# Kernel optimization log

Measured on AMD Instinct MI355X. Metric: run time of the kernel, lower is better.

## Reference

```python
import jax, jax.numpy as jnp
import numpy as np


def setup_inputs() -> dict:
    key = jax.random.key(0)
    k1, k2 = jax.random.split(key)
    x = jax.random.normal(k1, (4, 2048, 512), dtype=jnp.float32)
    proxy = jax.random.normal(k2, (16, 512), dtype=jnp.float32)
    return {"x": x, "proxy": proxy}


def reference(x, proxy):
    # x: (B, S, D), proxy: (P, D)
    num_proxies = proxy.shape[0]
    # prods: (B, P, S) = proxy @ x^T per batch
    prods = jnp.einsum('pd,bsd->bps', proxy, x)
    # broadcast outer product: (B, P, S, D), then running prefix sum over seq
    y = jnp.cumsum(prods[..., None] * x[:, None, :, :], axis=2)
    # softmax gate over proxies (dim=1), scaled by sqrt(P)
    w = jax.nn.softmax(prods / jnp.sqrt(jnp.float32(num_proxies)), axis=1)
    # weighted sum over proxies -> (B, S, D)
    out = jnp.einsum('bps,bpsd->bsd', w, y)
    return out
```

## Files before the change

### kernel.cpp

```cpp
#include <hip/hip_runtime.h>
#include <hip/hip_bf16.h>

#define B 4
#define S 2048
#define D 512
#define P 16
#define NC 64
#define CL 32

__global__ __launch_bounds__(512) void k_pt(const float* __restrict__ x,
                                            const float* __restrict__ proxy,
                                            float* __restrict__ prods,
                                            float* __restrict__ wgt,
                                            float* __restrict__ T) {
    __shared__ float s_pr[CL][P];
    __shared__ float s_w [CL][P];

    const int c    = blockIdx.x & (NC - 1);
    const int b    = blockIdx.x >> 6;
    const int tid  = threadIdx.x;
    const int lane = tid & 63;
    const int wv   = tid >> 6;
    const int bs0  = b * S + c * CL;

    {
        float4 pA[P], pB[P];
#pragma unroll
        for (int p = 0; p < P; ++p) {
            const float* pr = proxy + p * D + lane * 8;
            pA[p] = *(const float4*)pr;
            pB[p] = *(const float4*)(pr + 4);
        }

#pragma unroll
        for (int r = 0; r < 4; ++r) {
            const int sl = wv * 4 + r;
            const int bs = bs0 + sl;
            const float* xr = x + (size_t)bs * D + lane * 8;
            float4 xa = *(const float4*)xr;
            float4 xb = *(const float4*)(xr + 4);

            float part[P];
#pragma unroll
            for (int p = 0; p < P; ++p) {
                part[p] = xa.x*pA[p].x + xa.y*pA[p].y + xa.z*pA[p].z + xa.w*pA[p].w
                        + xb.x*pB[p].x + xb.y*pB[p].y + xb.z*pB[p].z + xb.w*pB[p].w;
            }

            float a8[8];
#pragma unroll
            for (int k = 0; k < 8; ++k) {
                bool hi = lane & 1;
                float mine = hi ? part[2*k+1] : part[2*k];
                float oth  = hi ? part[2*k]   : part[2*k+1];
                a8[k] = mine + __shfl_xor(oth, 1);
            }
            float a4[4];
#pragma unroll
            for (int k = 0; k < 4; ++k) {
                bool hi = lane & 2;
                float mine = hi ? a8[2*k+1] : a8[2*k];
                float oth  = hi ? a8[2*k]   : a8[2*k+1];
                a4[k] = mine + __shfl_xor(oth, 2);
            }
            float a2[2];
#pragma unroll
            for (int k = 0; k < 2; ++k) {
                bool hi = lane & 4;
                float mine = hi ? a4[2*k+1] : a4[2*k];
                float oth  = hi ? a4[2*k]   : a4[2*k+1];
                a2[k] = mine + __shfl_xor(oth, 4);
            }
            float a1;
            {
                bool hi = lane & 8;
                float mine = hi ? a2[1] : a2[0];
                float oth  = hi ? a2[0] : a2[1];
                a1 = mine + __shfl_xor(oth, 8);
            }
            a1 += __shfl_xor(a1, 16);
            a1 += __shfl_xor(a1, 32);

            float m = a1;
#pragma unroll
            for (int off = 1; off < 16; off <<= 1) m = fmaxf(m, __shfl_xor(m, off));
            float e = __expf((a1 - m) * 0.25f);
            float den = e;
#pragma unroll
            for (int off = 1; off < 16; off <<= 1) den += __shfl_xor(den, off);

            if (lane < P) {
                float w = e / den;
                s_pr[sl][lane] = a1;
                s_w [sl][lane] = w;
                prods[(size_t)bs * P + lane] = a1;
                wgt  [(size_t)bs * P + lane] = w;
            }
        }
    }
    __syncthreads();

    {
        const int d = tid;
        float xv[CL];
#pragma unroll
        for (int i = 0; i < CL; ++i) xv[i] = x[(size_t)(bs0 + i) * D + d];

        float acc[P];
#pragma unroll
        for (int p = 0; p < P; ++p) acc[p] = 0.f;

#pragma unroll
        for (int i = 0; i < CL; ++i) {
            float pr[P];
            const float4* sp = (const float4*)&s_pr[i][0];
            ((float4*)pr)[0] = sp[0];
            ((float4*)pr)[1] = sp[1];
            ((float4*)pr)[2] = sp[2];
            ((float4*)pr)[3] = sp[3];
#pragma unroll
            for (int p = 0; p < P; ++p) acc[p] = fmaf(pr[p], xv[i], acc[p]);
        }
        size_t tb = (size_t)blockIdx.x * (P * D) + d;
#pragma unroll
        for (int p = 0; p < P; ++p) T[tb + p * D] = acc[p];
    }
}

__global__ __launch_bounds__(256) void k_scan(float* __restrict__ T) {
    int t = blockIdx.x * blockDim.x + threadIdx.x;
    int d = t & (D - 1);
    int p = (t >> 9) & (P - 1);
    int b = t >> 13;
    size_t base = ((size_t)b * NC * P + p) * D + d;
    float run = 0.f;
#pragma unroll 8
    for (int c = 0; c < NC; ++c) {
        size_t idx = base + (size_t)c * (P * D);
        float v = T[idx];
        T[idx] = run;
        run += v;
    }
}

__global__ __launch_bounds__(256) void k_apply(const float* __restrict__ x,
                                               const float* __restrict__ prods,
                                               const float* __restrict__ wgt,
                                               const float* __restrict__ T,
                                               float* __restrict__ out) {
    __shared__ float s_pw[2][CL][P];

    int h = blockIdx.x & 1;
    int c = (blockIdx.x >> 1) & (NC - 1);
    int b = blockIdx.x >> 7;
    int d = h * 256 + threadIdx.x;
    int bs0 = b * S + c * CL;

    {
        int t = threadIdx.x;
        if (t < 128) {
            ((float4*)&s_pw[0][0][0])[t] =
                ((const float4*)(prods + (size_t)bs0 * P))[t];
        } else {
            ((float4*)&s_pw[1][0][0])[t - 128] =
                ((const float4*)(wgt + (size_t)bs0 * P))[t - 128];
        }
    }

    float xv[CL];
#pragma unroll
    for (int i = 0; i < CL; ++i) xv[i] = x[(size_t)(bs0 + i) * D + d];

    float st[P];
    size_t tb = ((size_t)(b * NC + c)) * (P * D) + d;
#pragma unroll
    for (int p = 0; p < P; ++p) st[p] = T[tb + p * D];

    __syncthreads();

#pragma unroll
    for (int i = 0; i < CL; ++i) {
        float pr[P], ww[P];
        const float4* sp = (const float4*)&s_pw[0][i][0];
        const float4* sw = (const float4*)&s_pw[1][i][0];
        ((float4*)pr)[0] = sp[0];
        ((float4*)pr)[1] = sp[1];
        ((float4*)pr)[2] = sp[2];
        ((float4*)pr)[3] = sp[3];
        ((float4*)ww)[0] = sw[0];
        ((float4*)ww)[1] = sw[1];
        ((float4*)ww)[2] = sw[2];
        ((float4*)ww)[3] = sw[3];
        float o = 0.f;
#pragma unroll
        for (int p = 0; p < P; ++p) {
            st[p] = fmaf(pr[p], xv[i], st[p]);
            o = fmaf(ww[p], st[p], o);
        }
        out[(size_t)(bs0 + i) * D + d] = o;
    }
}

extern "C" void kernel_launch(void* const* d_in, const int* in_sizes, int n_in,
                              void* d_out, int out_size, void* d_ws, size_t ws_size,
                              hipStream_t stream) {
    const float* x     = (const float*)d_in[0];
    const float* proxy = (const float*)d_in[1];
    float* out   = (float*)d_out;

    float* prods = (float*)d_ws;
    float* wgt   = prods + (size_t)B * S * P;
    float* T     = wgt   + (size_t)B * S * P;

    k_pt   <<<B * NC,             512, 0, stream>>>(x, proxy, prods, wgt, T);
    k_scan <<<(B * P * D) / 256,  256, 0, stream>>>(T);
    k_apply<<<B * NC * 2,         256, 0, stream>>>(x, prods, wgt, T, out);
}
```

Baseline: 36.01 us.

## Fuse three kernels into one cooperative kernel with flag-based chunk prefix

Merges the projection/softmax, scan, and apply kernels into a single cooperative kernel. Each block publishes its chunk aggregate and sets a release flag. It then waits on the flags of all earlier chunks in the same batch and sums their aggregates directly, rather than relying on a separate scan pass. This removes two launches and the round-trips of prods, weights and x through global memory. In exchange, later chunks redo O(c) aggregate reads (quadratic total traffic), add spin-wait latency, and add a memset plus cooperative launch overhead.

```diff
diff --git a/kernel.cpp b/kernel.cpp
--- a/kernel.cpp
+++ b/kernel.cpp
@@ -8,16 +8,16 @@
 #define NC 64
 #define CL 32
 
-__global__ __launch_bounds__(512) void k_pt(const float* __restrict__ x,
-                                            const float* __restrict__ proxy,
-                                            float* __restrict__ prods,
-                                            float* __restrict__ wgt,
-                                            float* __restrict__ T) {
+__global__ __launch_bounds__(512) void k_fused(const float* __restrict__ x,
+                                               const float* __restrict__ proxy,
+                                               float* __restrict__ Tagg,
+                                               int* __restrict__ flag,
+                                               float* __restrict__ out) {
     __shared__ float s_pr[CL][P];
     __shared__ float s_w [CL][P];
 
-    const int c    = blockIdx.x & (NC - 1);
-    const int b    = blockIdx.x >> 6;
+    const int c    = blockIdx.x >> 2;
+    const int b    = blockIdx.x & 3;
     const int tid  = threadIdx.x;
     const int lane = tid & 63;
     const int wv   = tid >> 6;
@@ -90,22 +90,19 @@
             for (int off = 1; off < 16; off <<= 1) den += __shfl_xor(den, off);
 
             if (lane < P) {
-                float w = e / den;
                 s_pr[sl][lane] = a1;
-                s_w [sl][lane] = w;
-                prods[(size_t)bs * P + lane] = a1;
-                wgt  [(size_t)bs * P + lane] = w;
+                s_w [sl][lane] = e / den;
             }
         }
     }
     __syncthreads();
 
+    const int d = tid;
+    float xv[CL];
+#pragma unroll
+    for (int i = 0; i < CL; ++i) xv[i] = x[(size_t)(bs0 + i) * D + d];
+
     {
-        const int d = tid;
-        float xv[CL];
-#pragma unroll
-        for (int i = 0; i < CL; ++i) xv[i] = x[(size_t)(bs0 + i) * D + d];
-
         float acc[P];
 #pragma unroll
         for (int p = 0; p < P; ++p) acc[p] = 0.f;
@@ -121,68 +118,42 @@
 #pragma unroll
             for (int p = 0; p < P; ++p) acc[p] = fmaf(pr[p], xv[i], acc[p]);
         }
-        size_t tb = (size_t)blockIdx.x * (P * D) + d;
+        size_t tb = ((size_t)(b * NC + c)) * (P * D) + d;
 #pragma unroll
-        for (int p = 0; p < P; ++p) T[tb + p * D] = acc[p];
+        for (int p = 0; p < P; ++p) Tagg[tb + p * D] = acc[p];
     }
-}
+    __syncthreads();
+    if (tid == 0)
+        __hip_atomic_store(&flag[blockIdx.x], 1, __ATOMIC_RELEASE,
+                           __HIP_MEMORY_SCOPE_AGENT);
 
-__global__ __launch_bounds__(256) void k_scan(float* __restrict__ T) {
-    int t = blockIdx.x * blockDim.x + threadIdx.x;
-    int d = t & (D - 1);
-    int p = (t >> 9) & (P - 1);
-    int b = t >> 13;
-    size_t base = ((size_t)b * NC * P + p) * D + d;
-    float run = 0.f;
-#pragma unroll 8
-    for (int c = 0; c < NC; ++c) {
-        size_t idx = base + (size_t)c * (P * D);
-        float v = T[idx];
-        T[idx] = run;
-        run += v;
-    }
-}
+    float st[P];
+#pragma unroll
+    for (int p = 0; p < P; ++p) st[p] = 0.f;
 
-__global__ __launch_bounds__(256) void k_apply(const float* __restrict__ x,
-                                               const float* __restrict__ prods,
-                                               const float* __restrict__ wgt,
-                                               const float* __restrict__ T,
-                                               float* __restrict__ out) {
-    __shared__ float s_pw[2][CL][P];
+    if (c > 0) {
+        if (tid < c) {
+            while (__hip_atomic_load(&flag[(tid << 2) | b], __ATOMIC_RELAXED,
+                                     __HIP_MEMORY_SCOPE_AGENT) == 0)
+                __builtin_amdgcn_s_sleep(2);
+        }
+        __syncthreads();
+        (void)__hip_atomic_load(&flag[((c - 1) << 2) | b], __ATOMIC_ACQUIRE,
+                                __HIP_MEMORY_SCOPE_AGENT);
 
-    int h = blockIdx.x & 1;
-    int c = (blockIdx.x >> 1) & (NC - 1);
-    int b = blockIdx.x >> 7;
-    int d = h * 256 + threadIdx.x;
-    int bs0 = b * S + c * CL;
-
-    {
-        int t = threadIdx.x;
-        if (t < 128) {
-            ((float4*)&s_pw[0][0][0])[t] =
-                ((const float4*)(prods + (size_t)bs0 * P))[t];
-        } else {
-            ((float4*)&s_pw[1][0][0])[t - 128] =
-                ((const float4*)(wgt + (size_t)bs0 * P))[t - 128];
+#pragma unroll 4
+        for (int cc = 0; cc < c; ++cc) {
+            size_t ta = ((size_t)(b * NC + cc)) * (P * D) + d;
+#pragma unroll
+            for (int p = 0; p < P; ++p) st[p] += Tagg[ta + p * D];
         }
     }
-
-    float xv[CL];
-#pragma unroll
-    for (int i = 0; i < CL; ++i) xv[i] = x[(size_t)(bs0 + i) * D + d];
-
-    float st[P];
-    size_t tb = ((size_t)(b * NC + c)) * (P * D) + d;
-#pragma unroll
-    for (int p = 0; p < P; ++p) st[p] = T[tb + p * D];
-
-    __syncthreads();
 
 #pragma unroll
     for (int i = 0; i < CL; ++i) {
         float pr[P], ww[P];
-        const float4* sp = (const float4*)&s_pw[0][i][0];
-        const float4* sw = (const float4*)&s_pw[1][i][0];
+        const float4* sp = (const float4*)&s_pr[i][0];
+        const float4* sw = (const float4*)&s_w [i][0];
         ((float4*)pr)[0] = sp[0];
         ((float4*)pr)[1] = sp[1];
         ((float4*)pr)[2] = sp[2];
@@ -206,13 +177,16 @@
                               hipStream_t stream) {
     const float* x     = (const float*)d_in[0];
     const float* proxy = (const float*)d_in[1];
-    float* out   = (float*)d_out;
+    float* out  = (float*)d_out;
 
-    float* prods = (float*)d_ws;
-    float* wgt   = prods + (size_t)B * S * P;
-    float* T     = wgt   + (size_t)B * S * P;
+    float* Tagg = (float*)d_ws;
+    int*   flags = (int*)((char*)d_ws +
+                          (size_t)B * NC * P * D * sizeof(float));
 
-    k_pt   <<<B * NC,             512, 0, stream>>>(x, proxy, prods, wgt, T);
-    k_scan <<<(B * P * D) / 256,  256, 0, stream>>>(T);
-    k_apply<<<B * NC * 2,         256, 0, stream>>>(x, prods, wgt, T, out);
+    hipMemsetAsync(flags, 0, (B * NC) * sizeof(int), stream);
+
+    void* args[] = { (void*)&x, (void*)&proxy, (void*)&Tagg,
+                     (void*)&flags, (void*)&out };
+    hipLaunchCooperativeKernel((void*)k_fused, dim3(B * NC), dim3(512),
+                               args, 0, stream);
 }
```

After: 90.79 us. 152% more time.
